# Kernel tuning notes

Measured on AMD Instinct MI355X. Metric: run time of the kernel, lower is better.

The kernel has to match this reference:

```python
import jax, jax.numpy as jnp
import numpy as np

N = 10000          # num nodes == num_api
C = 128            # api_embed_channels
E = 320000         # num edges


def _mlp(x, w1, b1, w2, b2):
    # MLP.forward: elu(fc1) -> dropout(eval: identity) -> elu(fc2). BN method is never called.
    return jax.nn.elu(jax.nn.elu(x @ w1 + b1) @ w2 + b2)


def setup_inputs() -> dict:
    key = jax.random.key(0)
    ks = jax.random.split(key, 24)
    r = lambda i, shape, s: (jax.random.normal(ks[i], shape, jnp.float32) * s)
    d = {}
    d['api_embeds'] = r(0, (N, C), 1.0)
    d['adjacency_matrix'] = jax.random.uniform(ks[1], (N, N), jnp.float32)
    d['edge_index'] = jax.random.randint(ks[2], (2, E), 0, N, jnp.int64)
    # reduce_mlp (dead code in original forward, kept for signature parity)
    d['w_red1'] = r(3, (N, 3 * C), 0.01);  d['b_red1'] = jnp.full((3 * C,), 0.1, jnp.float32)
    d['w_red2'] = r(4, (3 * C, C), 0.05);  d['b_red2'] = jnp.full((C,), 0.1, jnp.float32)
    # Node2Node.mlp1: MLP(4C, 2C, 2C)
    d['w_m1a'] = r(5, (4 * C, 2 * C), 0.05); d['b_m1a'] = jnp.full((2 * C,), 0.1, jnp.float32)
    d['w_m1b'] = r(6, (2 * C, 2 * C), 0.05); d['b_m1b'] = jnp.full((2 * C,), 0.1, jnp.float32)
    # Node2Node.mlp2: MLP(2C, 2C, 2C)
    d['w_m2a'] = r(7, (2 * C, 2 * C), 0.05); d['b_m2a'] = jnp.full((2 * C,), 0.1, jnp.float32)
    d['w_m2b'] = r(8, (2 * C, 2 * C), 0.05); d['b_m2b'] = jnp.full((2 * C,), 0.1, jnp.float32)
    # AdaptiveNRI.mlp: MLP(2C, 2C, 2C)
    d['w_ma'] = r(9, (2 * C, 2 * C), 0.05);  d['b_ma'] = jnp.full((2 * C,), 0.1, jnp.float32)
    d['w_mb'] = r(10, (2 * C, 2 * C), 0.05); d['b_mb'] = jnp.full((2 * C,), 0.1, jnp.float32)
    # increase_mlp: Linear(C, 3C) -> ReLU -> Linear(3C, N) -> Sigmoid
    d['w_inc1'] = r(11, (C, 3 * C), 0.05);   d['b_inc1'] = jnp.full((3 * C,), 0.1, jnp.float32)
    d['w_inc2'] = r(12, (3 * C, N), 0.05);   d['b_inc2'] = jnp.full((N,), 0.1, jnp.float32)
    return d


def reference(api_embeds, adjacency_matrix, edge_index,
              w_red1, b_red1, w_red2, b_red2,
              w_m1a, b_m1a, w_m1b, b_m1b,
              w_m2a, b_m2a, w_m2b, b_m2b,
              w_ma, b_ma, w_mb, b_mb,
              w_inc1, b_inc1, w_inc2, b_inc2):
    # NOTE: in the original torch code, reduce_mlp(adjacency_matrix) is computed and
    # immediately overwritten (dead code) -> adjacency does not affect the output.
    x = jnp.concatenate([api_embeds, api_embeds], axis=1)          # [N, 2C]
    src = edge_index[0]   # x_j (source)
    dst = edge_index[1]   # x_i (target, aggregation index)
    # message: MLP1(cat[x_i, x_j]) per edge -> [E, 2C]
    msg = _mlp(jnp.concatenate([x[dst], x[src]], axis=-1), w_m1a, b_m1a, w_m1b, b_m1b)
    # aggregate: scatter-add at targets
    agg = jax.ops.segment_sum(msg, dst, num_segments=N)            # [N, 2C]
    # update: MLP2
    h = _mlp(agg, w_m2a, b_m2a, w_m2b, b_m2b)                      # [N, 2C]
    h = _mlp(h, w_ma, b_ma, w_mb, b_mb)                            # [N, 2C]
    h = h[:, -C:]                                                  # [N, C]
    out = jax.nn.sigmoid(jax.nn.relu(h @ w_inc1 + b_inc1) @ w_inc2 + b_inc2)  # [N, N]
    return out
```

## Files before the change

kernel.cpp:

```cpp
#include <hip/hip_runtime.h>

#define DEVI __device__ __forceinline__

typedef __attribute__((ext_vector_type(8))) short short8;
typedef __attribute__((ext_vector_type(4))) short short4v;
typedef __attribute__((ext_vector_type(4))) float f32x4;
typedef unsigned short u16;
typedef unsigned int u32;

DEVI float b2f(u16 u) { u32 x = ((u32)u) << 16; return __builtin_bit_cast(float, x); }
DEVI u16 f2b(float f) {
    u32 u = __builtin_bit_cast(u32, f);
    u32 r = u + 0x7FFFu + ((u >> 16) & 1u);
    return (u16)(r >> 16);
}
DEVI float eluf(float v) { return v > 0.f ? v : __expf(v) - 1.f; }

DEVI void gl16(const void* g, void* l) {
    __builtin_amdgcn_global_load_lds(
        (const __attribute__((address_space(1))) u32*)g,
        (__attribute__((address_space(3))) u32*)l, 16, 0, 0);
}

__global__ void k_convert(const float* __restrict__ in, u16* __restrict__ out, int n) {
    int i = blockIdx.x * blockDim.x + threadIdx.x;
    int stride = gridDim.x * blockDim.x;
    for (int j = i; j * 8 < n; j += stride) {
        int base = j * 8;
        if (base + 8 <= n) {
            float4 a = *(const float4*)(in + base);
            float4 b = *(const float4*)(in + base + 4);
            short8 o;
            o[0] = (short)f2b(a.x); o[1] = (short)f2b(a.y);
            o[2] = (short)f2b(a.z); o[3] = (short)f2b(a.w);
            o[4] = (short)f2b(b.x); o[5] = (short)f2b(b.y);
            o[6] = (short)f2b(b.z); o[7] = (short)f2b(b.w);
            *(short8*)(out + base) = o;
        } else {
            for (int t = base; t < n; ++t) out[t] = f2b(in[t]);
        }
    }
}

__global__ void k_wct(const float* __restrict__ w, u16* __restrict__ wct) {
    int t = blockIdx.x * 256 + threadIdx.x;
    if (t >= 512 * 128) return;
    int k = t & 127, j = t >> 7;
    float v;
    if (j < 256) v = w[k * 256 + j] + w[(k + 128) * 256 + j];
    else { int jj = j - 256; v = w[(k + 256) * 256 + jj] + w[(k + 384) * 256 + jj]; }
    wct[j * 128 + k] = f2b(v);
}

__global__ void k_tc(const float* __restrict__ w, u16* __restrict__ wt,
                     int K, int N, int Nalloc) {
    __shared__ float tile[32][33];
    int tx = threadIdx.x, ty = threadIdx.y;
    int k0 = blockIdx.y * 32, n0 = blockIdx.x * 32;
#pragma unroll
    for (int yy = 0; yy < 4; ++yy) {
        int k = k0 + ty + yy * 8, n = n0 + tx;
        tile[ty + yy * 8][tx] = (k < K && n < N) ? w[(size_t)k * N + n] : 0.f;
    }
    __syncthreads();
#pragma unroll
    for (int yy = 0; yy < 4; ++yy) {
        int n = n0 + ty + yy * 8, k = k0 + tx;
        if (n < Nalloc && k < K) wt[(size_t)n * K + k] = f2b(tile[tx][ty + yy * 8]);
    }
}

__global__ void k_hist(const int* __restrict__ ei, int* __restrict__ hist, int E) {
    int i = blockIdx.x * 256 + threadIdx.x;
    if (i < E) atomicAdd(&hist[ei[E + i]], 1);
}

__global__ void k_scan(const int* __restrict__ hist, int* __restrict__ cursor, int NB) {
    __shared__ int part[256];
    int t = threadIdx.x;
    int base = t * 40;
    int s = 0;
    for (int i = 0; i < 40; ++i) { int idx = base + i; if (idx < NB) s += hist[idx]; }
    part[t] = s;
    __syncthreads();
    if (t == 0) { int run = 0; for (int i = 0; i < 256; ++i) { int x = part[i]; part[i] = run; run += x; } }
    __syncthreads();
    int run = part[t];
    for (int i = 0; i < 40; ++i) {
        int idx = base + i;
        if (idx < NB) { int h = hist[idx]; cursor[idx] = run; run += h; }
    }
}

__global__ void k_scatter(const int* __restrict__ ei, int* __restrict__ cursor,
                          int* __restrict__ sdst, int* __restrict__ ssrc, int E) {
    int i = blockIdx.x * 256 + threadIdx.x;
    if (i >= E) return;
    int d = ei[E + i], s = ei[i];
    int pos = atomicAdd(&cursor[d], 1);
    sdst[pos] = d;
    ssrc[pos] = s;
}

__global__ __launch_bounds__(256, 2)
void k_gemm(const u16* __restrict__ A, const u16* __restrict__ BT,
            void* __restrict__ Cv, int M, int N, int K, int lda, int ldbt, int ldc) {
    __shared__ short lsA[128 * 64];
    __shared__ short lsB[128 * 64];
    const int tid = threadIdx.x, wave = tid >> 6, lane = tid & 63;
    const int m0 = blockIdx.y * 128, n0 = blockIdx.x * 128;
    const int wm = wave >> 1, wn = wave & 1;
    const int rowA = lane >> 3, colA = (lane & 7) * 8;

    f32x4 acc[4][4] = {};

    const int kch = K >> 6;
    for (int kc = 0; kc < kch; ++kc) {
#pragma unroll
        for (int i = 0; i < 4; ++i) {
            int slot = wave * 4 + i;
            const u16* ga = A + (size_t)(m0 + slot * 8 + rowA) * lda + kc * 64 + colA;
            gl16(ga, &lsA[slot * 512]);
            const u16* gb = BT + (size_t)(n0 + slot * 8 + rowA) * ldbt + kc * 64 + colA;
            gl16(gb, &lsB[slot * 512]);
        }
        __syncthreads();
#pragma unroll
        for (int ks = 0; ks < 2; ++ks) {
            short8 a[4], b[4];
#pragma unroll
            for (int m = 0; m < 4; ++m)
                a[m] = *(const short8*)&lsA[(wm * 64 + m * 16 + (lane & 15)) * 64 + ks * 32 + (lane >> 4) * 8];
#pragma unroll
            for (int n = 0; n < 4; ++n)
                b[n] = *(const short8*)&lsB[(wn * 64 + n * 16 + (lane & 15)) * 64 + ks * 32 + (lane >> 4) * 8];
#pragma unroll
            for (int m = 0; m < 4; ++m)
#pragma unroll
                for (int n = 0; n < 4; ++n)
                    acc[m][n] = __builtin_amdgcn_mfma_f32_16x16x32_bf16(a[m], b[n], acc[m][n], 0, 0, 0);
        }
        __syncthreads();
    }

#pragma unroll
    for (int m = 0; m < 4; ++m) {
#pragma unroll
        for (int n = 0; n < 4; ++n) {
            int colg = n0 + wn * 64 + n * 16 + (lane & 15);
#pragma unroll
            for (int j = 0; j < 4; ++j) {
                int rowg = m0 + wm * 64 + m * 16 + (lane >> 4) * 4 + j;
                if (rowg < M && colg < N)
                    ((u16*)Cv)[(size_t)rowg * ldc + colg] = f2b(acc[m][n][j]);
            }
        }
    }
}

__global__ __launch_bounds__(512, 4)
void k_gemm2(const u16* __restrict__ A, const u16* __restrict__ BT,
             const float* __restrict__ bias, float* __restrict__ C,
             int M, int N, int K, int lda, int ldbt, int ldc, int NBX) {
    __shared__ short lsA[256 * 64];
    __shared__ short lsB[128 * 64];
    const int tid = threadIdx.x, wave = tid >> 6, lane = tid & 63;
    const int g = lane >> 4, l15 = lane & 15;
    const int nb = gridDim.x, orig = blockIdx.x;
    const int cpx = nb >> 3;
    const int wg = (orig & 7) * cpx + (orig >> 3);
    const int bx = wg % NBX, by = wg / NBX;
    const int m0 = by * 256, n0 = bx * 128;
    const int wm = wave >> 1, wn = wave & 1;
    const int sr = lane >> 3, sc = lane & 7;

    f32x4 acc[4][4] = {};
    const int kch = K >> 6;
    for (int kc = 0; kc < kch; ++kc) {
#pragma unroll
        for (int i = 0; i < 4; ++i) {
            int s = wave * 4 + i;
            int br = s * 8 + sr;
            const u16* ga = A + (size_t)(m0 + br) * lda + kc * 64 + ((sc ^ (br & 7)) * 8);
            gl16(ga, &lsA[s * 512]);
        }
#pragma unroll
        for (int i = 0; i < 2; ++i) {
            int s = wave * 2 + i;
            int br = s * 8 + sr;
            const u16* gb = BT + (size_t)(n0 + br) * ldbt + kc * 64 + ((sc ^ (br & 7)) * 8);
            gl16(gb, &lsB[s * 512]);
        }
        __syncthreads();
#pragma unroll
        for (int ks = 0; ks < 2; ++ks) {
            short8 a[4], b[4];
#pragma unroll
            for (int m = 0; m < 4; ++m) {
                int ar = wm * 64 + m * 16 + l15;
                a[m] = *(const short8*)&lsA[(ar * 8 + ((ks * 4 + g) ^ (ar & 7))) * 8];
            }
#pragma unroll
            for (int n = 0; n < 4; ++n) {
                int br = wn * 64 + n * 16 + l15;
                b[n] = *(const short8*)&lsB[(br * 8 + ((ks * 4 + g) ^ (br & 7))) * 8];
            }
#pragma unroll
            for (int m = 0; m < 4; ++m)
#pragma unroll
                for (int n = 0; n < 4; ++n)
                    acc[m][n] = __builtin_amdgcn_mfma_f32_16x16x32_bf16(b[n], a[m], acc[m][n], 0, 0, 0);
        }
        __syncthreads();
    }

#pragma unroll
    for (int m = 0; m < 4; ++m) {
        int row = m0 + wm * 64 + m * 16 + l15;
        if (row < M) {
#pragma unroll
            for (int n = 0; n < 4; ++n) {
                int col0 = n0 + wn * 64 + n * 16 + g * 4;
                if (col0 < N) {
                    float4 bv = *(const float4*)(bias + col0);
                    f32x4 o;
                    o[0] = 1.f / (1.f + __expf(-(acc[m][n][0] + bv.x)));
                    o[1] = 1.f / (1.f + __expf(-(acc[m][n][1] + bv.y)));
                    o[2] = 1.f / (1.f + __expf(-(acc[m][n][2] + bv.z)));
                    o[3] = 1.f / (1.f + __expf(-(acc[m][n][3] + bv.w)));
                    __builtin_nontemporal_store(o, (f32x4*)(C + (size_t)row * ldc + col0));
                }
            }
        }
    }
}

__global__ __launch_bounds__(256, 2)
void k_chain(const float* __restrict__ agg,
             const u16* __restrict__ w2aT, const float* __restrict__ b_m2a,
             const u16* __restrict__ w2bT, const float* __restrict__ b_m2b,
             const u16* __restrict__ waT,  const float* __restrict__ b_ma,
             const u16* __restrict__ wbT,  const float* __restrict__ b_mb,
             const u16* __restrict__ i1T,  const float* __restrict__ b_inc1,
             u16* __restrict__ H1, int M) {
    __shared__ short lsX[32 * 256];
    __shared__ short lsW[384 * 64];
    const int tid = threadIdx.x, wave = tid >> 6, lane = tid & 63;
    const int g = lane >> 4, l15 = lane & 15;
    const int r0 = blockIdx.x * 32;

    for (int c = tid; c < 2048; c += 256) {
        int row = c >> 6, cg = c & 63;
        int grow = r0 + row;
        float4 v = (grow < M) ? *(const float4*)(agg + (size_t)grow * 256 + cg * 4)
                              : float4{0.f, 0.f, 0.f, 0.f};
        short4v o;
        o[0] = (short)f2b(v.x); o[1] = (short)f2b(v.y);
        o[2] = (short)f2b(v.z); o[3] = (short)f2b(v.w);
        *(short4v*)&lsX[row * 256 + (((cg >> 1) ^ (row & 7)) * 8 + (cg & 1) * 4)] = o;
    }

    auto do_layer = [&](const u16* WT, const float* bias) {
        f32x4 acc[2][4] = {};
        for (int kc = 0; kc < 4; ++kc) {
#pragma unroll
            for (int i = 0; i < 8; ++i) {
                int slot = wave * 8 + i;
                int br = slot * 8 + (lane >> 3);
                const u16* gw = WT + (size_t)br * 256 + kc * 64 + (((lane & 7) ^ (br & 7)) * 8);
                gl16(gw, &lsW[slot * 512]);
            }
            __syncthreads();
#pragma unroll
            for (int ks = 0; ks < 2; ++ks) {
                short8 a[2], b[4];
#pragma unroll
                for (int m = 0; m < 2; ++m) {
                    int ar = m * 16 + l15;
                    a[m] = *(const short8*)&lsX[ar * 256 + (kc * 8 + ((ks * 4 + g) ^ (ar & 7))) * 8];
                }
#pragma unroll
                for (int n = 0; n < 4; ++n) {
                    int br = wave * 64 + n * 16 + l15;
                    b[n] = *(const short8*)&lsW[(br * 8 + ((ks * 4 + g) ^ (br & 7))) * 8];
                }
#pragma unroll
                for (int m = 0; m < 2; ++m)
#pragma unroll
                    for (int n = 0; n < 4; ++n)
                        acc[m][n] = __builtin_amdgcn_mfma_f32_16x16x32_bf16(b[n], a[m], acc[m][n], 0, 0, 0);
            }
            __syncthreads();
        }
#pragma unroll
        for (int m = 0; m < 2; ++m) {
#pragma unroll
            for (int n = 0; n < 4; ++n) {
                int row = m * 16 + l15;
                int col0 = wave * 64 + n * 16 + g * 4;
                float4 bv = *(const float4*)(bias + col0);
                short4v o;
                o[0] = (short)f2b(eluf(acc[m][n][0] + bv.x));
                o[1] = (short)f2b(eluf(acc[m][n][1] + bv.y));
                o[2] = (short)f2b(eluf(acc[m][n][2] + bv.z));
                o[3] = (short)f2b(eluf(acc[m][n][3] + bv.w));
                int cg = col0 >> 2;
                *(short4v*)&lsX[row * 256 + (((cg >> 1) ^ (row & 7)) * 8 + (cg & 1) * 4)] = o;
            }
        }
        __syncthreads();
    };

    do_layer(w2aT, b_m2a);
    do_layer(w2bT, b_m2b);
    do_layer(waT,  b_ma);
    do_layer(wbT,  b_mb);

    f32x4 acc2[2][6] = {};
    for (int kc = 0; kc < 2; ++kc) {
#pragma unroll
        for (int i = 0; i < 12; ++i) {
            int slot = wave * 12 + i;
            int br = slot * 8 + (lane >> 3);
            const u16* gw = i1T + (size_t)br * 128 + kc * 64 + (((lane & 7) ^ (br & 7)) * 8);
            gl16(gw, &lsW[slot * 512]);
        }
        __syncthreads();
#pragma unroll
        for (int ks = 0; ks < 2; ++ks) {
            short8 a[2], b[6];
#pragma unroll
            for (int m = 0; m < 2; ++m) {
                int ar = m * 16 + l15;
                a[m] = *(const short8*)&lsX[ar * 256 + (16 + kc * 8 + ((ks * 4 + g) ^ (ar & 7))) * 8];
            }
#pragma unroll
            for (int n = 0; n < 6; ++n) {
                int br = wave * 96 + n * 16 + l15;
                b[n] = *(const short8*)&lsW[(br * 8 + ((ks * 4 + g) ^ (br & 7))) * 8];
            }
#pragma unroll
            for (int m = 0; m < 2; ++m)
#pragma unroll
                for (int n = 0; n < 6; ++n)
                    acc2[m][n] = __builtin_amdgcn_mfma_f32_16x16x32_bf16(b[n], a[m], acc2[m][n], 0, 0, 0);
        }
        __syncthreads();
    }
#pragma unroll
    for (int m = 0; m < 2; ++m) {
        int grow = r0 + m * 16 + l15;
        if (grow < M) {
#pragma unroll
            for (int n = 0; n < 6; ++n) {
                int col0 = wave * 96 + n * 16 + g * 4;
                float4 bv = *(const float4*)(b_inc1 + col0);
                float v0 = acc2[m][n][0] + bv.x, v1 = acc2[m][n][1] + bv.y;
                float v2 = acc2[m][n][2] + bv.z, v3 = acc2[m][n][3] + bv.w;
                short4v o;
                o[0] = (short)f2b(v0 > 0.f ? v0 : 0.f);
                o[1] = (short)f2b(v1 > 0.f ? v1 : 0.f);
                o[2] = (short)f2b(v2 > 0.f ? v2 : 0.f);
                o[3] = (short)f2b(v3 > 0.f ? v3 : 0.f);
                *(short4v*)&H1[(size_t)grow * 384 + col0] = o;
            }
        }
    }
}

__global__ __launch_bounds__(256, 2)
void k_edge(const u16* __restrict__ P, const int* __restrict__ sdst,
            const int* __restrict__ ssrc, const float* __restrict__ b1,
            const u16* __restrict__ W2T, const float* __restrict__ b2,
            float* __restrict__ agg) {
    __shared__ __align__(16) char smem[49152];
    __shared__ int dstl[128];
    __shared__ int srcl[128];
    short* lsA = (short*)smem;
    short* lsB = (short*)(smem + 16384);
    float* lsO = (float*)smem;
    const int tid = threadIdx.x, wave = tid >> 6, lane = tid & 63;
    const int eb = blockIdx.x * 128;
    const int g = lane >> 4, l15 = lane & 15;

    if (tid < 128) srcl[tid] = ssrc[eb + tid];
    else dstl[tid - 128] = sdst[eb + (tid - 128)];
    __syncthreads();

    short8 rpd[4], rps[4];
    auto loadA = [&](int kc) {
#pragma unroll
        for (int it = 0; it < 4; ++it) {
            int chunk = it * 256 + tid;
            int r = chunk >> 3, cc = chunk & 7;
            int col = kc * 64 + cc * 8;
            rpd[it] = *(const short8*)(P + (size_t)dstl[r] * 512 + col);
            rps[it] = *(const short8*)(P + (size_t)srcl[r] * 512 + 256 + col);
        }
    };

    loadA(0);
    f32x4 acc[4][2][4] = {};

    for (int kc = 0; kc < 4; ++kc) {
#pragma unroll
        for (int it = 0; it < 4; ++it) {
            int chunk = it * 256 + tid;
            int r = chunk >> 3, cc = chunk & 7;
            int col = kc * 64 + cc * 8;
            float bv[8];
            *(float4*)&bv[0] = *(const float4*)(b1 + col);
            *(float4*)&bv[4] = *(const float4*)(b1 + col + 4);
            short8 o;
#pragma unroll
            for (int jj = 0; jj < 8; ++jj) {
                float v = b2f((u16)rpd[it][jj]) + b2f((u16)rps[it][jj]) + bv[jj];
                o[jj] = (short)f2b(eluf(v));
            }
            int ccs = cc ^ (r & 7);
            *(short8*)&lsA[(r * 8 + ccs) * 8] = o;
        }
#pragma unroll
        for (int i = 0; i < 8; ++i) {
            int br = (wave * 8 + i) * 8 + (lane >> 3);
            const u16* gb = W2T + (size_t)br * 256 + kc * 64 + (((lane & 7) ^ (br & 7)) * 8);
            gl16(gb, lsB + (wave * 8 + i) * 512);
        }
        __syncthreads();
        if (kc < 3) loadA(kc + 1);
#pragma unroll
        for (int nq = 0; nq < 4; ++nq) {
#pragma unroll
            for (int ks = 0; ks < 2; ++ks) {
                short8 a[2], b[4];
#pragma unroll
                for (int m = 0; m < 2; ++m) {
                    int ar = wave * 32 + m * 16 + l15;
                    a[m] = *(const short8*)&lsA[(ar * 8 + ((ks * 4 + g) ^ (ar & 7))) * 8];
                }
#pragma unroll
                for (int n = 0; n < 4; ++n) {
                    int br = nq * 64 + n * 16 + l15;
                    b[n] = *(const short8*)&lsB[(br * 8 + ((ks * 4 + g) ^ (br & 7))) * 8];
                }
#pragma unroll
                for (int m = 0; m < 2; ++m)
#pragma unroll
                    for (int n = 0; n < 4; ++n)
                        acc[nq][m][n] = __builtin_amdgcn_mfma_f32_16x16x32_bf16(a[m], b[n], acc[nq][m][n], 0, 0, 0);
            }
        }
        __syncthreads();
    }

    const int r0w = wave * 32;
    const int dls = dstl[r0w + (lane & 31)];

#pragma unroll
    for (int nq = 0; nq < 4; ++nq) {
        float b2v[4];
#pragma unroll
        for (int n = 0; n < 4; ++n) b2v[n] = b2[nq * 64 + n * 16 + l15];
#pragma unroll
        for (int m = 0; m < 2; ++m)
#pragma unroll
            for (int n = 0; n < 4; ++n)
#pragma unroll
                for (int j = 0; j < 4; ++j) {
                    int row = r0w + m * 16 + g * 4 + j;
                    lsO[row * 68 + n * 16 + l15] = eluf(acc[nq][m][n][j] + b2v[n]);
                }
        __syncthreads();
        {
            int dprev = __builtin_amdgcn_readlane(dls, 0);
            float sum = 0.f;
#pragma unroll
            for (int i = 0; i < 32; ++i) {
                int d = __builtin_amdgcn_readlane(dls, i);
                float v = lsO[(r0w + i) * 68 + lane];
                if (d != dprev) {
                    atomicAdd(&agg[(size_t)dprev * 256 + nq * 64 + lane], sum);
                    sum = v; dprev = d;
                } else sum += v;
            }
            atomicAdd(&agg[(size_t)dprev * 256 + nq * 64 + lane], sum);
        }
        __syncthreads();
    }
}

extern "C" void kernel_launch(void* const* d_in, const int* in_sizes, int n_in,
                              void* d_out, int out_size, void* d_ws, size_t ws_size,
                              hipStream_t stream) {
    const float* api    = (const float*)d_in[0];
    const int*   ei     = (const int*)d_in[2];
    const float* w_m1a  = (const float*)d_in[7];
    const float* b_m1a  = (const float*)d_in[8];
    const float* w_m1b  = (const float*)d_in[9];
    const float* b_m1b  = (const float*)d_in[10];
    const float* w_m2a  = (const float*)d_in[11];
    const float* b_m2a  = (const float*)d_in[12];
    const float* w_m2b  = (const float*)d_in[13];
    const float* b_m2b  = (const float*)d_in[14];
    const float* w_ma   = (const float*)d_in[15];
    const float* b_ma   = (const float*)d_in[16];
    const float* w_mb   = (const float*)d_in[17];
    const float* b_mb   = (const float*)d_in[18];
    const float* w_inc1 = (const float*)d_in[19];
    const float* b_inc1 = (const float*)d_in[20];
    const float* w_inc2 = (const float*)d_in[21];
    const float* b_inc2 = (const float*)d_in[22];

    const int N = 10000, C = 128, E = 320000, Mp = 10112;
    const int Mp2 = 10240;

    char* w = (char*)d_ws;
    size_t off = 0;
    auto alloc = [&](size_t bytes) { void* p = w + off; off += (bytes + 255) & ~(size_t)255; return p; };
    u16* e16   = (u16*)alloc((size_t)Mp * 128 * 2);
    u16* WcT   = (u16*)alloc(512 * 128 * 2);
    u16* P     = (u16*)alloc((size_t)Mp * 512 * 2);
    u16* w1bT  = (u16*)alloc(256 * 256 * 2);
    u16* w2aT  = (u16*)alloc(256 * 256 * 2);
    u16* w2bT  = (u16*)alloc(256 * 256 * 2);
    u16* waT   = (u16*)alloc(256 * 256 * 2);
    u16* wbT   = (u16*)alloc(256 * 256 * 2);
    u16* i1T   = (u16*)alloc(384 * 128 * 2);
    u16* i2T   = (u16*)alloc((size_t)Mp2 * 384 * 2);
    float* agg = (float*)alloc((size_t)N * 256 * 4);
    u16* H1    = (u16*)alloc((size_t)Mp2 * 384 * 2);
    int* hist  = (int*)alloc((size_t)N * 4);
    int* cursor= (int*)alloc((size_t)N * 4);
    int* sdst  = (int*)alloc((size_t)E * 4);
    int* ssrc  = (int*)alloc((size_t)E * 4);
    (void)ws_size; (void)in_sizes; (void)n_in; (void)out_size;

    dim3 tb(32, 8);
    hipMemsetAsync(hist, 0, (size_t)N * 4, stream);
    k_hist<<<1250, 256, 0, stream>>>(ei, hist, E);
    k_scan<<<1, 256, 0, stream>>>(hist, cursor, N);
    k_scatter<<<1250, 256, 0, stream>>>(ei, cursor, sdst, ssrc, E);

    k_convert<<<640, 256, 0, stream>>>(api, e16, N * C);
    k_wct<<<256, 256, 0, stream>>>(w_m1a, WcT);
    k_tc<<<dim3(8, 8),  tb, 0, stream>>>(w_m1b,  w1bT, 256, 256, 256);
    k_tc<<<dim3(8, 8),  tb, 0, stream>>>(w_m2a,  w2aT, 256, 256, 256);
    k_tc<<<dim3(8, 8),  tb, 0, stream>>>(w_m2b,  w2bT, 256, 256, 256);
    k_tc<<<dim3(8, 8),  tb, 0, stream>>>(w_ma,   waT,  256, 256, 256);
    k_tc<<<dim3(8, 8),  tb, 0, stream>>>(w_mb,   wbT,  256, 256, 256);
    k_tc<<<dim3(12, 4), tb, 0, stream>>>(w_inc1, i1T,  128, 384, 384);
    k_tc<<<dim3(320, 12), tb, 0, stream>>>(w_inc2, i2T, 384, 10000, Mp2);
    hipMemsetAsync(agg, 0, (size_t)N * 256 * 4, stream);

    k_gemm<<<dim3(4, 79), 256, 0, stream>>>(e16, WcT, P, N, 512, 128, 128, 128, 512);
    k_edge<<<2500, 256, 0, stream>>>(P, sdst, ssrc, b_m1a, w1bT, b_m1b, agg);
    k_chain<<<313, 256, 0, stream>>>(agg, w2aT, b_m2a, w2bT, b_m2b,
                                     waT, b_ma, wbT, b_mb, i1T, b_inc1, H1, N);
    k_gemm2<<<40 * 79, 512, 0, stream>>>(H1, i2T, b_inc2, (float*)d_out,
                                         N, 10000, 384, 384, 384, 10000, 79);
}
```

Measured before the change: 403.8 us.

## Remap GEMM2 tile order per XCD, fuse weight transposes, trim edge-kernel syncs

Replaces the output GEMM's block-to-tile mapping with a hardcoded per-XCD grouping of 5 row tiles by 8 column tiles, so concurrently running blocks share A and B panels in cache. Merges five 256x256 weight transposes into one launch using blockIdx.z. In the edge kernel it loads A fragments once per k-chunk instead of once per output quarter, and drops two block barriers around the per-wave LDS reduction, which relies on each wave touching only its own rows. The remap hardcodes grid dimensions for this problem size.

```diff
diff --git a/kernel.cpp b/kernel.cpp
--- a/kernel.cpp
+++ b/kernel.cpp
@@ -70,6 +70,31 @@
     }
 }
 
+__global__ void k_tc5(const float* __restrict__ w0, const float* __restrict__ w1,
+                      const float* __restrict__ w2, const float* __restrict__ w3,
+                      const float* __restrict__ w4,
+                      u16* __restrict__ t0, u16* __restrict__ t1, u16* __restrict__ t2,
+                      u16* __restrict__ t3, u16* __restrict__ t4) {
+    __shared__ float tile[32][33];
+    const float* w; u16* wt;
+    switch (blockIdx.z) {
+        case 0: w = w0; wt = t0; break;
+        case 1: w = w1; wt = t1; break;
+        case 2: w = w2; wt = t2; break;
+        case 3: w = w3; wt = t3; break;
+        default: w = w4; wt = t4; break;
+    }
+    int tx = threadIdx.x, ty = threadIdx.y;
+    int k0 = blockIdx.y * 32, n0 = blockIdx.x * 32;
+#pragma unroll
+    for (int yy = 0; yy < 4; ++yy)
+        tile[ty + yy * 8][tx] = w[(size_t)(k0 + ty + yy * 8) * 256 + n0 + tx];
+    __syncthreads();
+#pragma unroll
+    for (int yy = 0; yy < 4; ++yy)
+        wt[(size_t)(n0 + ty + yy * 8) * 256 + k0 + tx] = f2b(tile[tx][ty + yy * 8]);
+}
+
 __global__ void k_hist(const int* __restrict__ ei, int* __restrict__ hist, int E) {
     int i = blockIdx.x * 256 + threadIdx.x;
     if (i < E) atomicAdd(&hist[ei[E + i]], 1);
@@ -161,18 +186,22 @@
 __global__ __launch_bounds__(512, 4)
 void k_gemm2(const u16* __restrict__ A, const u16* __restrict__ BT,
              const float* __restrict__ bias, float* __restrict__ C,
-             int M, int N, int K, int lda, int ldbt, int ldc, int NBX) {
+             int M, int N, int K, int lda, int ldbt, int ldc) {
     __shared__ short lsA[256 * 64];
     __shared__ short lsB[128 * 64];
     const int tid = threadIdx.x, wave = tid >> 6, lane = tid & 63;
     const int g = lane >> 4, l15 = lane & 15;
-    const int nb = gridDim.x, orig = blockIdx.x;
-    const int cpx = nb >> 3;
-    const int wg = (orig & 7) * cpx + (orig >> 3);
-    const int bx = wg % NBX, by = wg / NBX;
+    const int orig = blockIdx.x;
+    const int wg = (orig & 7) * 395 + (orig >> 3);
+    const int x = wg / 395;
+    const int l = wg - x * 395;
+    int bxl, byl;
+    if (l < 360) { int sc = l / 40, r = l - sc * 40; int q = r / 5; bxl = sc * 8 + q; byl = r - q * 5; }
+    else         { int r = l - 360;                   int q = r / 5; bxl = 72 + q;     byl = r - q * 5; }
+    const int bx = bxl, by = x * 5 + byl;
     const int m0 = by * 256, n0 = bx * 128;
     const int wm = wave >> 1, wn = wave & 1;
-    const int sr = lane >> 3, sc = lane & 7;
+    const int sr = lane >> 3, sc2 = lane & 7;
 
     f32x4 acc[4][4] = {};
     const int kch = K >> 6;
@@ -181,14 +210,14 @@
         for (int i = 0; i < 4; ++i) {
             int s = wave * 4 + i;
             int br = s * 8 + sr;
-            const u16* ga = A + (size_t)(m0 + br) * lda + kc * 64 + ((sc ^ (br & 7)) * 8);
+            const u16* ga = A + (size_t)(m0 + br) * lda + kc * 64 + ((sc2 ^ (br & 7)) * 8);
             gl16(ga, &lsA[s * 512]);
         }
 #pragma unroll
         for (int i = 0; i < 2; ++i) {
             int s = wave * 2 + i;
             int br = s * 8 + sr;
-            const u16* gb = BT + (size_t)(n0 + br) * ldbt + kc * 64 + ((sc ^ (br & 7)) * 8);
+            const u16* gb = BT + (size_t)(n0 + br) * ldbt + kc * 64 + ((sc2 ^ (br & 7)) * 8);
             gl16(gb, &lsB[s * 512]);
         }
         __syncthreads();
@@ -428,16 +457,19 @@
         }
         __syncthreads();
         if (kc < 3) loadA(kc + 1);
+        short8 af[2][2];
+#pragma unroll
+        for (int ks = 0; ks < 2; ++ks)
+#pragma unroll
+            for (int m = 0; m < 2; ++m) {
+                int ar = wave * 32 + m * 16 + l15;
+                af[ks][m] = *(const short8*)&lsA[(ar * 8 + ((ks * 4 + g) ^ (ar & 7))) * 8];
+            }
 #pragma unroll
         for (int nq = 0; nq < 4; ++nq) {
 #pragma unroll
             for (int ks = 0; ks < 2; ++ks) {
-                short8 a[2], b[4];
-#pragma unroll
-                for (int m = 0; m < 2; ++m) {
-                    int ar = wave * 32 + m * 16 + l15;
-                    a[m] = *(const short8*)&lsA[(ar * 8 + ((ks * 4 + g) ^ (ar & 7))) * 8];
-                }
+                short8 b[4];
 #pragma unroll
                 for (int n = 0; n < 4; ++n) {
                     int br = nq * 64 + n * 16 + l15;
@@ -447,7 +479,7 @@
                 for (int m = 0; m < 2; ++m)
 #pragma unroll
                     for (int n = 0; n < 4; ++n)
-                        acc[nq][m][n] = __builtin_amdgcn_mfma_f32_16x16x32_bf16(a[m], b[n], acc[nq][m][n], 0, 0, 0);
+                        acc[nq][m][n] = __builtin_amdgcn_mfma_f32_16x16x32_bf16(af[ks][m], b[n], acc[nq][m][n], 0, 0, 0);
             }
         }
         __syncthreads();
@@ -470,7 +502,6 @@
                     int row = r0w + m * 16 + g * 4 + j;
                     lsO[row * 68 + n * 16 + l15] = eluf(acc[nq][m][n][j] + b2v[n]);
                 }
-        __syncthreads();
         {
             int dprev = __builtin_amdgcn_readlane(dls, 0);
             float sum = 0.f;
@@ -485,7 +516,6 @@
             }
             atomicAdd(&agg[(size_t)dprev * 256 + nq * 64 + lane], sum);
         }
-        __syncthreads();
     }
 }
 
@@ -543,11 +573,8 @@
 
     k_convert<<<640, 256, 0, stream>>>(api, e16, N * C);
     k_wct<<<256, 256, 0, stream>>>(w_m1a, WcT);
-    k_tc<<<dim3(8, 8),  tb, 0, stream>>>(w_m1b,  w1bT, 256, 256, 256);
-    k_tc<<<dim3(8, 8),  tb, 0, stream>>>(w_m2a,  w2aT, 256, 256, 256);
-    k_tc<<<dim3(8, 8),  tb, 0, stream>>>(w_m2b,  w2bT, 256, 256, 256);
-    k_tc<<<dim3(8, 8),  tb, 0, stream>>>(w_ma,   waT,  256, 256, 256);
-    k_tc<<<dim3(8, 8),  tb, 0, stream>>>(w_mb,   wbT,  256, 256, 256);
+    k_tc5<<<dim3(8, 8, 5), tb, 0, stream>>>(w_m1b, w_m2a, w_m2b, w_ma, w_mb,
+                                            w1bT, w2aT, w2bT, waT, wbT);
     k_tc<<<dim3(12, 4), tb, 0, stream>>>(w_inc1, i1T,  128, 384, 384);
     k_tc<<<dim3(320, 12), tb, 0, stream>>>(w_inc2, i2T, 384, 10000, Mp2);
     hipMemsetAsync(agg, 0, (size_t)N * 256 * 4, stream);
@@ -556,6 +583,6 @@
     k_edge<<<2500, 256, 0, stream>>>(P, sdst, ssrc, b_m1a, w1bT, b_m1b, agg);
     k_chain<<<313, 256, 0, stream>>>(agg, w2aT, b_m2a, w2bT, b_m2b,
                                      waT, b_ma, wbT, b_mb, i1T, b_inc1, H1, N);
-    k_gemm2<<<40 * 79, 512, 0, stream>>>(H1, i2T, b_inc2, (float*)d_out,
-                                         N, 10000, 384, 384, 384, 10000, 79);
-}
+    k_gemm2<<<3160, 512, 0, stream>>>(H1, i2T, b_inc2, (float*)d_out,
+                                      N, 10000, 384, 384, 384, 10000);
+}
```

After: 389.2 us. 3.6% less time.
